# Kernel tuning notes

Measured on AMD Instinct MI355X. Metric: run time of the kernel, lower is better.

The kernel has to match this reference:

```python
import jax, jax.numpy as jnp
import numpy as np

DIM = 1024

def setup_inputs() -> dict:
    key = jax.random.key(0)
    k1, k2, k3, k4 = jax.random.split(key, 4)
    scale = 1.0 / np.sqrt(DIM)
    return {
        "segment_embeds": jax.random.normal(k1, (32, 2048, DIM), dtype=jnp.float32),
        "Wq": jax.random.normal(k2, (DIM, DIM), dtype=jnp.float32) * scale,
        "bq": jax.random.normal(k3, (DIM,), dtype=jnp.float32) * scale,
        "mem_bank": jax.random.normal(k4, (131072, DIM), dtype=jnp.float32) * scale,
        "k": 8,
    }

def reference(segment_embeds, Wq, bq, mem_bank, k):
    # mean-pool over time: (B, C)
    segment_mean = segment_embeds.mean(axis=1)
    # linear query projection (torch Linear: x @ W.T + b)
    q = segment_mean @ Wq.T + bq
    # dense scores against memory bank: (B, M)
    attn_scores = (q @ mem_bank.T) / jnp.sqrt(jnp.asarray(DIM, dtype=q.dtype))
    # top-k select
    top_k_scores, top_k_indices = jax.lax.top_k(attn_scores, k)  # (B, K)
    attn_weights = jax.nn.softmax(top_k_scores, axis=-1)  # (B, K)
    # gather retrieved vectors: (B, K, C)
    retrieved_vectors = mem_bank[top_k_indices]
    # weighted sum over K, keepdim -> (B, 1, C)
    retrieved_mem = jnp.sum(attn_weights[..., None] * retrieved_vectors, axis=1, keepdims=True)
    return retrieved_mem
```

## Files before the change

### kernel.cpp

```cpp
#include <hip/hip_runtime.h>
#include <hip/hip_bf16.h>
#include <math.h>

#define NB 32
#define NT 2048
#define NC 1024
#define NM 131072
#define TOPK 8
#define MBLK 128
#define SBLOCKS (NM / MBLK)

typedef __attribute__((ext_vector_type(8))) short s16x8;
typedef __attribute__((ext_vector_type(4))) float f32x4;
typedef __attribute__((ext_vector_type(4))) int i32x4;

#define OFF_PART 0
#define OFF_CS   0
#define OFF_CI   262144
#define OFF_MEAN 1048576
#define OFF_Q    (OFF_MEAN + 32768)
#define OFF_QB   (OFF_Q + 32768)

__device__ __forceinline__ unsigned short f2bf(float f) {
    unsigned u = __float_as_uint(f);
    unsigned r = (u + 0x7FFFu + ((u >> 16) & 1u)) >> 16;
    return (unsigned short)r;
}

__global__ __launch_bounds__(256) void mean_partial_k(const float* __restrict__ seg,
                                                      float* __restrict__ part) {
    int blk = blockIdx.x;
    int b = blk >> 5, tc = blk & 31;
    int tid = threadIdx.x;
    const float4* src = (const float4*)(seg + ((size_t)b * NT + (size_t)tc * 64) * NC);
    float4 acc = make_float4(0.f, 0.f, 0.f, 0.f);
#pragma unroll 4
    for (int t = 0; t < 64; ++t) {
        float4 v = src[(size_t)t * 256 + tid];
        acc.x += v.x; acc.y += v.y; acc.z += v.z; acc.w += v.w;
    }
    ((float4*)(part + ((size_t)b * 32 + tc) * NC))[tid] = acc;
}

__global__ __launch_bounds__(256) void mean_finalize_k(const float* __restrict__ part,
                                                       float* __restrict__ mean) {
    int i = blockIdx.x * 256 + threadIdx.x;
    int b = i >> 10, c = i & 1023;
    float s = 0.f;
#pragma unroll
    for (int tc = 0; tc < 32; ++tc) s += part[((size_t)b * 32 + tc) * NC + c];
    mean[i] = s * (1.0f / NT);
}

__global__ __launch_bounds__(256) void qproj_k(const float* __restrict__ mean,
                                               const float* __restrict__ Wq,
                                               const float* __restrict__ bq,
                                               float* __restrict__ q) {
    int wave = (blockIdx.x * 256 + threadIdx.x) >> 6;
    int lane = threadIdx.x & 63;
    int o0 = wave * 16;
    for (int j = 0; j < 16; ++j) {
        int o = o0 + j;
        int b = o >> 10, i = o & 1023;
        const float4* wr = (const float4*)(Wq + (size_t)i * NC);
        const float4* mr = (const float4*)(mean + (size_t)b * NC);
        float acc = 0.f;
#pragma unroll
        for (int e = 0; e < 4; ++e) {
            float4 w4 = wr[lane * 4 + e];
            float4 m4 = mr[lane * 4 + e];
            acc += w4.x * m4.x + w4.y * m4.y + w4.z * m4.z + w4.w * m4.w;
        }
#pragma unroll
        for (int off = 32; off; off >>= 1) acc += __shfl_xor(acc, off);
        if (lane == 0) q[o] = acc + bq[i];
    }
}

__global__ __launch_bounds__(256) void qbf_k(const float* __restrict__ q,
                                             s16x8* __restrict__ qb) {
    int idx = blockIdx.x * 256 + threadIdx.x;
    int lane = idx & 63, n = (idx >> 6) & 1, ks = idx >> 7;
    int b = n * 16 + (lane & 15);
    int k0 = ks * 32 + ((lane >> 4) << 3);
    s16x8 v;
#pragma unroll
    for (int e = 0; e < 8; ++e) v[e] = (short)f2bf(q[(size_t)b * NC + k0 + e]);
    qb[idx] = v;
}

#define BUBBLE8(v, vi, s, si)                                   \
    {                                                           \
        float _v = (v); int _vi = (vi);                         \
        _Pragma("unroll")                                       \
        for (int _u = 0; _u < 8; ++_u) {                        \
            bool _gt = _v > s[_u];                              \
            float _ts = _gt ? _v : s[_u];                       \
            int _ti = _gt ? _vi : si[_u];                       \
            _v = _gt ? s[_u] : _v;                              \
            _vi = _gt ? si[_u] : _vi;                           \
            s[_u] = _ts; si[_u] = _ti;                          \
        }                                                       \
    }

__global__ __launch_bounds__(256) void scores_mfma_k(const float* __restrict__ memb,
                                                     const s16x8* __restrict__ qb,
                                                     float* __restrict__ candS,
                                                     int* __restrict__ candI) {
    __shared__ __align__(16) float smemf[5760];
    int tid = threadIdx.x, lane = tid & 63, wid = tid >> 6;
    int m0 = blockIdx.x * MBLK;

    f32x4 acc[2][2];
#pragma unroll
    for (int t = 0; t < 2; ++t)
#pragma unroll
        for (int n = 0; n < 2; ++n)
            acc[t][n] = (f32x4){0.f, 0.f, 0.f, 0.f};

    const unsigned* abase = (const unsigned*)(memb
        + (size_t)(m0 + wid * 32 + (lane & 15)) * NC + ((lane >> 4) << 3));
    s16x8 bf0 = qb[0 * 64 + lane];
    s16x8 bf1 = qb[1 * 64 + lane];

    for (int ks = 0; ks < 32; ++ks) {
        s16x8 nb0, nb1;
        if (ks < 31) {
            nb0 = qb[((ks + 1) * 2 + 0) * 64 + lane];
            nb1 = qb[((ks + 1) * 2 + 1) * 64 + lane];
        }
#pragma unroll
        for (int t = 0; t < 2; ++t) {
            const unsigned* ap = abase + (size_t)(t * 16) * NC + ks * 32;
            uint4 lo = *(const uint4*)(ap);
            uint4 hi = *(const uint4*)(ap + 4);
            i32x4 ai;
            ai[0] = __builtin_amdgcn_perm(lo.y, lo.x, 0x07060302u);
            ai[1] = __builtin_amdgcn_perm(lo.w, lo.z, 0x07060302u);
            ai[2] = __builtin_amdgcn_perm(hi.y, hi.x, 0x07060302u);
            ai[3] = __builtin_amdgcn_perm(hi.w, hi.z, 0x07060302u);
            s16x8 a = __builtin_bit_cast(s16x8, ai);
            acc[t][0] = __builtin_amdgcn_mfma_f32_16x16x32_bf16(a, bf0, acc[t][0], 0, 0, 0);
            acc[t][1] = __builtin_amdgcn_mfma_f32_16x16x32_bf16(a, bf1, acc[t][1], 0, 0, 0);
        }
        bf0 = nb0; bf1 = nb1;
    }

#pragma unroll
    for (int t = 0; t < 2; ++t)
#pragma unroll
        for (int n = 0; n < 2; ++n)
#pragma unroll
            for (int j = 0; j < 4; ++j) {
                int bb = n * 16 + (lane & 15);
                int mm = wid * 32 + t * 16 + ((lane >> 4) << 2) + j;
                smemf[bb * 129 + mm] = acc[t][n][j] * 0.03125f;
            }
    __syncthreads();

    {
        int b = tid >> 3, p = tid & 7;
        float s[8]; int si[8];
#pragma unroll
        for (int u = 0; u < 8; ++u) { s[u] = -INFINITY; si[u] = -1; }
#pragma unroll
        for (int j = 0; j < 16; ++j) {
            int ml = (p + j * 8 + b * 4) & 127;
            float v = smemf[b * 129 + ml];
            BUBBLE8(v, m0 + ml, s, si);
        }
        __syncthreads();
        float* cs = smemf;
        int* ci = (int*)(smemf + 2304);
#pragma unroll
        for (int u = 0; u < 8; ++u) { cs[tid * 9 + u] = s[u]; ci[tid * 9 + u] = si[u]; }
        __syncthreads();
        float* csA = smemf + 4608;
        int* ciA = (int*)(smemf + 5184);
        if (tid < 64) {
            float s2[8]; int si2[8];
#pragma unroll
            for (int u = 0; u < 8; ++u) { s2[u] = -INFINITY; si2[u] = -1; }
            int t0 = (tid >> 1) * 8 + (tid & 1) * 4;
            for (int tt = 0; tt < 4; ++tt)
#pragma unroll
                for (int u = 0; u < 8; ++u)
                    BUBBLE8(cs[(t0 + tt) * 9 + u], ci[(t0 + tt) * 9 + u], s2, si2);
#pragma unroll
            for (int u = 0; u < 8; ++u) { csA[tid * 9 + u] = s2[u]; ciA[tid * 9 + u] = si2[u]; }
        }
        __syncthreads();
        if (tid < 32) {
            float s3[8]; int si3[8];
#pragma unroll
            for (int u = 0; u < 8; ++u) { s3[u] = -INFINITY; si3[u] = -1; }
            for (int j = 0; j < 16; ++j)
                BUBBLE8(csA[(tid * 2 + (j >> 3)) * 9 + (j & 7)],
                        ciA[(tid * 2 + (j >> 3)) * 9 + (j & 7)], s3, si3);
#pragma unroll
            for (int u = 0; u < 8; ++u) {
                candS[((size_t)tid * SBLOCKS + blockIdx.x) * 8 + u] = s3[u];
                candI[((size_t)tid * SBLOCKS + blockIdx.x) * 8 + u] = si3[u];
            }
        }
    }
}

__global__ __launch_bounds__(256) void finalize_k(const float* __restrict__ candS,
                                                  const int* __restrict__ candI,
                                                  const float* __restrict__ memb,
                                                  const float* __restrict__ q,
                                                  float* __restrict__ out) {
    __shared__ float cs[256 * 9];
    __shared__ int ci[256 * 9];
    __shared__ float csA[64 * 9];
    __shared__ int ciA[64 * 9];
    __shared__ float exsc[64];
    __shared__ int exid[64];
    __shared__ float wgt[8];
    __shared__ int widx[8];
    int b = blockIdx.x, tid = threadIdx.x;
    const float* S = candS + (size_t)b * (SBLOCKS * 8);
    const int* I = candI + (size_t)b * (SBLOCKS * 8);

    {
        float s[8]; int si[8];
#pragma unroll
        for (int u = 0; u < 8; ++u) { s[u] = -INFINITY; si[u] = -1; }
        for (int j = 0; j < 32; ++j)
            BUBBLE8(S[tid * 32 + j], I[tid * 32 + j], s, si);
#pragma unroll
        for (int u = 0; u < 8; ++u) { cs[tid * 9 + u] = s[u]; ci[tid * 9 + u] = si[u]; }
    }
    __syncthreads();
    if (tid < 64) {
        float s[8]; int si[8];
#pragma unroll
        for (int u = 0; u < 8; ++u) { s[u] = -INFINITY; si[u] = -1; }
        for (int tt = 0; tt < 4; ++tt)
#pragma unroll
            for (int u = 0; u < 8; ++u)
                BUBBLE8(cs[(tid * 4 + tt) * 9 + u], ci[(tid * 4 + tt) * 9 + u], s, si);
#pragma unroll
        for (int u = 0; u < 8; ++u) { csA[tid * 9 + u] = s[u]; ciA[tid * 9 + u] = si[u]; }
    }
    __syncthreads();
    if (tid < 8) {
        float s[8]; int si[8];
#pragma unroll
        for (int u = 0; u < 8; ++u) { s[u] = -INFINITY; si[u] = -1; }
        for (int tt = 0; tt < 8; ++tt)
#pragma unroll
            for (int u = 0; u < 8; ++u)
                BUBBLE8(csA[(tid * 8 + tt) * 9 + u], ciA[(tid * 8 + tt) * 9 + u], s, si);
#pragma unroll
        for (int u = 0; u < 8; ++u) exid[tid * 8 + u] = si[u];
    }
    __syncthreads();
    {
        int w = tid >> 6, lane = tid & 63;
        const float4* qr = (const float4*)(q + (size_t)b * NC);
        for (int i = 0; i < 16; ++i) {
            int c = w * 16 + i;
            int row = exid[c];
            const float4* mr = (const float4*)(memb + (size_t)row * NC);
            float d = 0.f;
#pragma unroll
            for (int e = 0; e < 4; ++e) {
                float4 m4 = mr[e * 64 + lane];
                float4 q4 = qr[e * 64 + lane];
                d += m4.x * q4.x + m4.y * q4.y + m4.z * q4.z + m4.w * q4.w;
            }
#pragma unroll
            for (int off = 32; off; off >>= 1) d += __shfl_xor(d, off);
            if (lane == 0) exsc[c] = d * 0.03125f;
        }
    }
    __syncthreads();
    if (tid == 0) {
        float s4[8]; int si4[8];
#pragma unroll
        for (int u = 0; u < 8; ++u) { s4[u] = -INFINITY; si4[u] = -1; }
        for (int j = 0; j < 64; ++j)
            BUBBLE8(exsc[j], exid[j], s4, si4);
        float m = s4[0], sum = 0.f, w[8];
#pragma unroll
        for (int u = 0; u < 8; ++u) { w[u] = __expf(s4[u] - m); sum += w[u]; }
        float inv = 1.0f / sum;
#pragma unroll
        for (int u = 0; u < 8; ++u) { wgt[u] = w[u] * inv; widx[u] = si4[u]; }
    }
    __syncthreads();
    {
        float wv[8]; int ix[8];
#pragma unroll
        for (int u = 0; u < 8; ++u) { wv[u] = wgt[u]; ix[u] = widx[u]; }
        float4 o = make_float4(0.f, 0.f, 0.f, 0.f);
#pragma unroll
        for (int u = 0; u < 8; ++u) {
            float4 r = ((const float4*)(memb + (size_t)ix[u] * NC))[tid];
            o.x = fmaf(wv[u], r.x, o.x);
            o.y = fmaf(wv[u], r.y, o.y);
            o.z = fmaf(wv[u], r.z, o.z);
            o.w = fmaf(wv[u], r.w, o.w);
        }
        ((float4*)(out + (size_t)b * NC))[tid] = o;
    }
}

extern "C" void kernel_launch(void* const* d_in, const int* in_sizes, int n_in,
                              void* d_out, int out_size, void* d_ws, size_t ws_size,
                              hipStream_t stream) {
    const float* seg  = (const float*)d_in[0];
    const float* Wq   = (const float*)d_in[1];
    const float* bq   = (const float*)d_in[2];
    const float* memb = (const float*)d_in[3];
    float* ws = (float*)d_ws;
    float* part  = ws + OFF_PART;
    float* mean  = ws + OFF_MEAN;
    float* q     = ws + OFF_Q;
    s16x8* qb    = (s16x8*)(ws + OFF_QB);
    float* candS = ws + OFF_CS;
    int*   candI = (int*)(ws + OFF_CI);
    float* out = (float*)d_out;

    mean_partial_k<<<NB * 32, 256, 0, stream>>>(seg, part);
    mean_finalize_k<<<(NB * NC) / 256, 256, 0, stream>>>(part, mean);
    qproj_k<<<512, 256, 0, stream>>>(mean, Wq, bq, q);
    qbf_k<<<16, 256, 0, stream>>>(q, qb);
    scores_mfma_k<<<SBLOCKS, 256, 0, stream>>>(memb, qb, candS, candI);
    finalize_k<<<NB, 256, 0, stream>>>(candS, candI, memb, q, out);
}
```

Measured before the change: 233.8 us.

## Halve score tile per block, pack indices into score bits, prefetch A loads

The scoring kernel now covers 64 memory rows per block instead of 128, with one 16-row MFMA tile per wave, and raises the occupancy hint to 8 blocks. The next k-step's memory-bank loads are prefetched into registers across iterations, using a scheduling barrier. The local row index is packed into the low 8 mantissa bits of each score, so the per-block top-8 selection sorts floats only and drops the parallel index arrays. This trades a tiny loss of score precision, which could change tie ordering, for fewer registers and less shared memory, while doubling the candidate count the finalize kernel has to merge.

```diff
diff --git a/kernel.cpp b/kernel.cpp
--- a/kernel.cpp
+++ b/kernel.cpp
@@ -7,7 +7,7 @@
 #define NC 1024
 #define NM 131072
 #define TOPK 8
-#define MBLK 128
+#define MBLK 64
 #define SBLOCKS (NM / MBLK)
 
 typedef __attribute__((ext_vector_type(8))) short s16x8;
@@ -16,7 +16,7 @@
 
 #define OFF_PART 0
 #define OFF_CS   0
-#define OFF_CI   262144
+#define OFF_CI   524288
 #define OFF_MEAN 1048576
 #define OFF_Q    (OFF_MEAN + 32768)
 #define OFF_QB   (OFF_Q + 32768)
@@ -103,104 +103,109 @@
         }                                                       \
     }
 
-__global__ __launch_bounds__(256) void scores_mfma_k(const float* __restrict__ memb,
-                                                     const s16x8* __restrict__ qb,
-                                                     float* __restrict__ candS,
-                                                     int* __restrict__ candI) {
-    __shared__ __align__(16) float smemf[5760];
+#define BUBBLE8F(v, s)                                          \
+    {                                                           \
+        float _v = (v);                                         \
+        _Pragma("unroll")                                       \
+        for (int _u = 0; _u < 8; ++_u) {                        \
+            bool _gt = _v > s[_u];                              \
+            float _ts = _gt ? _v : s[_u];                       \
+            _v = _gt ? s[_u] : _v;                              \
+            s[_u] = _ts;                                        \
+        }                                                       \
+    }
+
+__global__ __launch_bounds__(256, 8) void scores_mfma_k(const float* __restrict__ memb,
+                                                        const s16x8* __restrict__ qb,
+                                                        float* __restrict__ candS,
+                                                        int* __restrict__ candI) {
+    __shared__ __align__(16) float smemf[2880];
     int tid = threadIdx.x, lane = tid & 63, wid = tid >> 6;
     int m0 = blockIdx.x * MBLK;
 
-    f32x4 acc[2][2];
-#pragma unroll
-    for (int t = 0; t < 2; ++t)
-#pragma unroll
-        for (int n = 0; n < 2; ++n)
-            acc[t][n] = (f32x4){0.f, 0.f, 0.f, 0.f};
+    f32x4 acc[2];
+    acc[0] = (f32x4){0.f, 0.f, 0.f, 0.f};
+    acc[1] = (f32x4){0.f, 0.f, 0.f, 0.f};
 
     const unsigned* abase = (const unsigned*)(memb
-        + (size_t)(m0 + wid * 32 + (lane & 15)) * NC + ((lane >> 4) << 3));
-    s16x8 bf0 = qb[0 * 64 + lane];
-    s16x8 bf1 = qb[1 * 64 + lane];
+        + (size_t)(m0 + wid * 16 + (lane & 15)) * NC + ((lane >> 4) << 3));
+    uint4 lo0 = *(const uint4*)(abase);
+    uint4 hi0 = *(const uint4*)(abase + 4);
+    s16x8 bf0 = qb[lane];
+    s16x8 bf1 = qb[64 + lane];
 
     for (int ks = 0; ks < 32; ++ks) {
-        s16x8 nb0, nb1;
+        uint4 lo1, hi1; s16x8 nb0, nb1;
         if (ks < 31) {
+            lo1 = *(const uint4*)(abase + (ks + 1) * 32);
+            hi1 = *(const uint4*)(abase + (ks + 1) * 32 + 4);
             nb0 = qb[((ks + 1) * 2 + 0) * 64 + lane];
             nb1 = qb[((ks + 1) * 2 + 1) * 64 + lane];
         }
-#pragma unroll
-        for (int t = 0; t < 2; ++t) {
-            const unsigned* ap = abase + (size_t)(t * 16) * NC + ks * 32;
-            uint4 lo = *(const uint4*)(ap);
-            uint4 hi = *(const uint4*)(ap + 4);
-            i32x4 ai;
-            ai[0] = __builtin_amdgcn_perm(lo.y, lo.x, 0x07060302u);
-            ai[1] = __builtin_amdgcn_perm(lo.w, lo.z, 0x07060302u);
-            ai[2] = __builtin_amdgcn_perm(hi.y, hi.x, 0x07060302u);
-            ai[3] = __builtin_amdgcn_perm(hi.w, hi.z, 0x07060302u);
-            s16x8 a = __builtin_bit_cast(s16x8, ai);
-            acc[t][0] = __builtin_amdgcn_mfma_f32_16x16x32_bf16(a, bf0, acc[t][0], 0, 0, 0);
-            acc[t][1] = __builtin_amdgcn_mfma_f32_16x16x32_bf16(a, bf1, acc[t][1], 0, 0, 0);
-        }
-        bf0 = nb0; bf1 = nb1;
-    }
-
-#pragma unroll
-    for (int t = 0; t < 2; ++t)
-#pragma unroll
-        for (int n = 0; n < 2; ++n)
-#pragma unroll
-            for (int j = 0; j < 4; ++j) {
-                int bb = n * 16 + (lane & 15);
-                int mm = wid * 32 + t * 16 + ((lane >> 4) << 2) + j;
-                smemf[bb * 129 + mm] = acc[t][n][j] * 0.03125f;
-            }
+        __builtin_amdgcn_sched_barrier(0);
+        i32x4 ai;
+        ai[0] = __builtin_amdgcn_perm(lo0.y, lo0.x, 0x07060302u);
+        ai[1] = __builtin_amdgcn_perm(lo0.w, lo0.z, 0x07060302u);
+        ai[2] = __builtin_amdgcn_perm(hi0.y, hi0.x, 0x07060302u);
+        ai[3] = __builtin_amdgcn_perm(hi0.w, hi0.z, 0x07060302u);
+        s16x8 a = __builtin_bit_cast(s16x8, ai);
+        acc[0] = __builtin_amdgcn_mfma_f32_16x16x32_bf16(a, bf0, acc[0], 0, 0, 0);
+        acc[1] = __builtin_amdgcn_mfma_f32_16x16x32_bf16(a, bf1, acc[1], 0, 0, 0);
+        lo0 = lo1; hi0 = hi1; bf0 = nb0; bf1 = nb1;
+    }
+
+#pragma unroll
+    for (int n = 0; n < 2; ++n)
+#pragma unroll
+        for (int j = 0; j < 4; ++j) {
+            int bb = n * 16 + (lane & 15);
+            int mm = wid * 16 + ((lane >> 4) << 2) + j;
+            smemf[bb * 65 + mm] = acc[n][j] * 0.03125f;
+        }
     __syncthreads();
 
     {
         int b = tid >> 3, p = tid & 7;
-        float s[8]; int si[8];
-#pragma unroll
-        for (int u = 0; u < 8; ++u) { s[u] = -INFINITY; si[u] = -1; }
-#pragma unroll
-        for (int j = 0; j < 16; ++j) {
-            int ml = (p + j * 8 + b * 4) & 127;
-            float v = smemf[b * 129 + ml];
-            BUBBLE8(v, m0 + ml, s, si);
+        float s[8];
+#pragma unroll
+        for (int u = 0; u < 8; ++u) s[u] = -INFINITY;
+#pragma unroll
+        for (int j = 0; j < 8; ++j) {
+            int ml = (p + j * 8 + b * 4) & 63;
+            float v = smemf[b * 65 + ml];
+            unsigned uu = (__float_as_uint(v) & ~0xFFu) | (unsigned)ml;
+            BUBBLE8F(__uint_as_float(uu), s);
         }
         __syncthreads();
         float* cs = smemf;
-        int* ci = (int*)(smemf + 2304);
-#pragma unroll
-        for (int u = 0; u < 8; ++u) { cs[tid * 9 + u] = s[u]; ci[tid * 9 + u] = si[u]; }
+#pragma unroll
+        for (int u = 0; u < 8; ++u) cs[tid * 9 + u] = s[u];
         __syncthreads();
-        float* csA = smemf + 4608;
-        int* ciA = (int*)(smemf + 5184);
+        float* csA = smemf + 2304;
         if (tid < 64) {
-            float s2[8]; int si2[8];
-#pragma unroll
-            for (int u = 0; u < 8; ++u) { s2[u] = -INFINITY; si2[u] = -1; }
+            float s2[8];
+#pragma unroll
+            for (int u = 0; u < 8; ++u) s2[u] = -INFINITY;
             int t0 = (tid >> 1) * 8 + (tid & 1) * 4;
             for (int tt = 0; tt < 4; ++tt)
 #pragma unroll
                 for (int u = 0; u < 8; ++u)
-                    BUBBLE8(cs[(t0 + tt) * 9 + u], ci[(t0 + tt) * 9 + u], s2, si2);
-#pragma unroll
-            for (int u = 0; u < 8; ++u) { csA[tid * 9 + u] = s2[u]; ciA[tid * 9 + u] = si2[u]; }
+                    BUBBLE8F(cs[(t0 + tt) * 9 + u], s2);
+#pragma unroll
+            for (int u = 0; u < 8; ++u) csA[tid * 9 + u] = s2[u];
         }
         __syncthreads();
         if (tid < 32) {
-            float s3[8]; int si3[8];
-#pragma unroll
-            for (int u = 0; u < 8; ++u) { s3[u] = -INFINITY; si3[u] = -1; }
+            float s3[8];
+#pragma unroll
+            for (int u = 0; u < 8; ++u) s3[u] = -INFINITY;
             for (int j = 0; j < 16; ++j)
-                BUBBLE8(csA[(tid * 2 + (j >> 3)) * 9 + (j & 7)],
-                        ciA[(tid * 2 + (j >> 3)) * 9 + (j & 7)], s3, si3);
+                BUBBLE8F(csA[(tid * 2 + (j >> 3)) * 9 + (j & 7)], s3);
 #pragma unroll
             for (int u = 0; u < 8; ++u) {
                 candS[((size_t)tid * SBLOCKS + blockIdx.x) * 8 + u] = s3[u];
-                candI[((size_t)tid * SBLOCKS + blockIdx.x) * 8 + u] = si3[u];
+                candI[((size_t)tid * SBLOCKS + blockIdx.x) * 8 + u] =
+                    m0 + (int)(__float_as_uint(s3[u]) & 0xFFu);
             }
         }
     }
@@ -227,8 +232,8 @@
         float s[8]; int si[8];
 #pragma unroll
         for (int u = 0; u < 8; ++u) { s[u] = -INFINITY; si[u] = -1; }
-        for (int j = 0; j < 32; ++j)
-            BUBBLE8(S[tid * 32 + j], I[tid * 32 + j], s, si);
+        for (int j = 0; j < 64; ++j)
+            BUBBLE8(S[tid * 64 + j], I[tid * 64 + j], s, si);
 #pragma unroll
         for (int u = 0; u < 8; ++u) { cs[tid * 9 + u] = s[u]; ci[tid * 9 + u] = si[u]; }
     }
```

New measurement: 233.2 us. About the same (-0.3%).

## Restructure scores kernel into single-wave blocks with double-buffered LDS staging

Applied to the files above, without the earlier changes.

The memory-bank scoring kernel now runs as 1024 single-wavefront blocks. Each block walks 8 panels of 16 rows and double-buffers 16x256 float tiles into LDS with direct global-to-LDS loads, prefetching the next tile while the MFMAs run on the current one. Top-k is kept per lane across panels and merged with a shuffle instead of multi-stage shared-memory reductions with block barriers. The goal is to overlap the bank streaming with compute and drop the synchronization overhead. In exchange there is less parallelism per block, explicit vmcnt(0) waits that may serialize the loads, and q fragments re-read from global on every tile.

```diff
diff --git a/kernel.cpp b/kernel.cpp
--- a/kernel.cpp
+++ b/kernel.cpp
@@ -7,8 +7,9 @@
 #define NC 1024
 #define NM 131072
 #define TOPK 8
-#define MBLK 128
-#define SBLOCKS (NM / MBLK)
+#define PANELS 8
+#define NSB 1024
+#define SLOTF 260
 
 typedef __attribute__((ext_vector_type(8))) short s16x8;
 typedef __attribute__((ext_vector_type(4))) float f32x4;
@@ -25,6 +26,11 @@
     unsigned u = __float_as_uint(f);
     unsigned r = (u + 0x7FFFu + ((u >> 16) & 1u)) >> 16;
     return (unsigned short)r;
+}
+
+__device__ __forceinline__ void gl_lds16(const float* g, float* l) {
+    __builtin_amdgcn_global_load_lds((const __attribute__((address_space(1))) void*)g,
+                                     (__attribute__((address_space(3))) void*)l, 16, 0, 0);
 }
 
 __global__ __launch_bounds__(256) void mean_partial_k(const float* __restrict__ seg,
@@ -94,7 +100,7 @@
         float _v = (v); int _vi = (vi);                         \
         _Pragma("unroll")                                       \
         for (int _u = 0; _u < 8; ++_u) {                        \
-            bool _gt = _v > s[_u];                              \
+            bool _gt = _v > s[_u];                               \
             float _ts = _gt ? _v : s[_u];                       \
             int _ti = _gt ? _vi : si[_u];                       \
             _v = _gt ? s[_u] : _v;                              \
@@ -103,104 +109,98 @@
         }                                                       \
     }
 
-__global__ __launch_bounds__(256) void scores_mfma_k(const float* __restrict__ memb,
-                                                     const s16x8* __restrict__ qb,
-                                                     float* __restrict__ candS,
-                                                     int* __restrict__ candI) {
-    __shared__ __align__(16) float smemf[5760];
-    int tid = threadIdx.x, lane = tid & 63, wid = tid >> 6;
-    int m0 = blockIdx.x * MBLK;
-
-    f32x4 acc[2][2];
-#pragma unroll
-    for (int t = 0; t < 2; ++t)
-#pragma unroll
-        for (int n = 0; n < 2; ++n)
-            acc[t][n] = (f32x4){0.f, 0.f, 0.f, 0.f};
-
-    const unsigned* abase = (const unsigned*)(memb
-        + (size_t)(m0 + wid * 32 + (lane & 15)) * NC + ((lane >> 4) << 3));
-    s16x8 bf0 = qb[0 * 64 + lane];
-    s16x8 bf1 = qb[1 * 64 + lane];
-
-    for (int ks = 0; ks < 32; ++ks) {
-        s16x8 nb0, nb1;
-        if (ks < 31) {
-            nb0 = qb[((ks + 1) * 2 + 0) * 64 + lane];
-            nb1 = qb[((ks + 1) * 2 + 1) * 64 + lane];
-        }
-#pragma unroll
-        for (int t = 0; t < 2; ++t) {
-            const unsigned* ap = abase + (size_t)(t * 16) * NC + ks * 32;
-            uint4 lo = *(const uint4*)(ap);
-            uint4 hi = *(const uint4*)(ap + 4);
+__global__ __launch_bounds__(64) void scores_mfma_k(const float* __restrict__ memb,
+                                                    const s16x8* __restrict__ qb,
+                                                    float* __restrict__ candS,
+                                                    int* __restrict__ candI) {
+    __shared__ __align__(16) float tiles[2 * 16 * SLOTF];
+    __shared__ __align__(16) float sc[32 * 17];
+    int lane = threadIdx.x;
+    size_t mb0 = (size_t)blockIdx.x * (PANELS * 16);
+
+    float s8[8]; int i8[8];
+#pragma unroll
+    for (int u = 0; u < 8; ++u) { s8[u] = -INFINITY; i8[u] = -1; }
+
+#define TISSUE(t_) { int p_ = (t_) >> 2, c_ = (t_) & 3;                               \
+    const float* rb_ = memb + (mb0 + p_ * 16) * NC + c_ * 256 + lane * 4;             \
+    float* lb_ = tiles + ((t_) & 1) * (16 * SLOTF);                                   \
+    _Pragma("unroll") for (int i_ = 0; i_ < 16; ++i_)                                 \
+        gl_lds16(rb_ + (size_t)i_ * NC, lb_ + i_ * SLOTF); }
+
+    f32x4 acc0 = (f32x4){0.f, 0.f, 0.f, 0.f};
+    f32x4 acc1 = (f32x4){0.f, 0.f, 0.f, 0.f};
+
+    TISSUE(0);
+    for (int t = 0; t < PANELS * 4; ++t) {
+        int c = t & 3;
+        s16x8 qf[16];
+#pragma unroll
+        for (int k = 0; k < 8; ++k) {
+            qf[2 * k]     = qb[((c * 8 + k) * 2 + 0) * 64 + lane];
+            qf[2 * k + 1] = qb[((c * 8 + k) * 2 + 1) * 64 + lane];
+        }
+        asm volatile("s_waitcnt vmcnt(0)" ::: "memory");
+        __builtin_amdgcn_sched_barrier(0);
+        if (t + 1 < PANELS * 4) TISSUE(t + 1);
+
+        const float* lanebase = tiles + (t & 1) * (16 * SLOTF)
+                              + (lane & 15) * SLOTF + ((lane >> 4) << 3);
+#pragma unroll
+        for (int ks = 0; ks < 8; ++ks) {
+            uint4 lo = *(const uint4*)(lanebase + ks * 32);
+            uint4 hi = *(const uint4*)(lanebase + ks * 32 + 4);
             i32x4 ai;
             ai[0] = __builtin_amdgcn_perm(lo.y, lo.x, 0x07060302u);
             ai[1] = __builtin_amdgcn_perm(lo.w, lo.z, 0x07060302u);
             ai[2] = __builtin_amdgcn_perm(hi.y, hi.x, 0x07060302u);
             ai[3] = __builtin_amdgcn_perm(hi.w, hi.z, 0x07060302u);
             s16x8 a = __builtin_bit_cast(s16x8, ai);
-            acc[t][0] = __builtin_amdgcn_mfma_f32_16x16x32_bf16(a, bf0, acc[t][0], 0, 0, 0);
-            acc[t][1] = __builtin_amdgcn_mfma_f32_16x16x32_bf16(a, bf1, acc[t][1], 0, 0, 0);
-        }
-        bf0 = nb0; bf1 = nb1;
-    }
-
-#pragma unroll
-    for (int t = 0; t < 2; ++t)
-#pragma unroll
-        for (int n = 0; n < 2; ++n)
+            acc0 = __builtin_amdgcn_mfma_f32_16x16x32_bf16(a, qf[2 * ks], acc0, 0, 0, 0);
+            acc1 = __builtin_amdgcn_mfma_f32_16x16x32_bf16(a, qf[2 * ks + 1], acc1, 0, 0, 0);
+        }
+
+        if (c == 3) {
+            int p = t >> 2;
 #pragma unroll
             for (int j = 0; j < 4; ++j) {
-                int bb = n * 16 + (lane & 15);
-                int mm = wid * 32 + t * 16 + ((lane >> 4) << 2) + j;
-                smemf[bb * 129 + mm] = acc[t][n][j] * 0.03125f;
+                sc[(0 * 16 + (lane & 15)) * 17 + ((lane >> 4) << 2) + j] = acc0[j];
+                sc[(1 * 16 + (lane & 15)) * 17 + ((lane >> 4) << 2) + j] = acc1[j];
             }
-    __syncthreads();
+            asm volatile("s_waitcnt lgkmcnt(0)" ::: "memory");
+            __builtin_amdgcn_sched_barrier(0);
+            int b = lane >> 1, p2 = lane & 1;
+            int midx0 = mb0 + p * 16;
+#pragma unroll
+            for (int j = 0; j < 8; ++j) {
+                int m = ((b + j) & 7) + p2 * 8;
+                float v = sc[b * 17 + m];
+                BUBBLE8(v, midx0 + m, s8, i8);
+            }
+            asm volatile("s_waitcnt lgkmcnt(0)" ::: "memory");
+            __builtin_amdgcn_sched_barrier(0);
+            acc0 = (f32x4){0.f, 0.f, 0.f, 0.f};
+            acc1 = (f32x4){0.f, 0.f, 0.f, 0.f};
+        }
+    }
+#undef TISSUE
 
     {
-        int b = tid >> 3, p = tid & 7;
-        float s[8]; int si[8];
-#pragma unroll
-        for (int u = 0; u < 8; ++u) { s[u] = -INFINITY; si[u] = -1; }
-#pragma unroll
-        for (int j = 0; j < 16; ++j) {
-            int ml = (p + j * 8 + b * 4) & 127;
-            float v = smemf[b * 129 + ml];
-            BUBBLE8(v, m0 + ml, s, si);
-        }
-        __syncthreads();
-        float* cs = smemf;
-        int* ci = (int*)(smemf + 2304);
-#pragma unroll
-        for (int u = 0; u < 8; ++u) { cs[tid * 9 + u] = s[u]; ci[tid * 9 + u] = si[u]; }
-        __syncthreads();
-        float* csA = smemf + 4608;
-        int* ciA = (int*)(smemf + 5184);
-        if (tid < 64) {
-            float s2[8]; int si2[8];
-#pragma unroll
-            for (int u = 0; u < 8; ++u) { s2[u] = -INFINITY; si2[u] = -1; }
-            int t0 = (tid >> 1) * 8 + (tid & 1) * 4;
-            for (int tt = 0; tt < 4; ++tt)
-#pragma unroll
-                for (int u = 0; u < 8; ++u)
-                    BUBBLE8(cs[(t0 + tt) * 9 + u], ci[(t0 + tt) * 9 + u], s2, si2);
-#pragma unroll
-            for (int u = 0; u < 8; ++u) { csA[tid * 9 + u] = s2[u]; ciA[tid * 9 + u] = si2[u]; }
-        }
-        __syncthreads();
-        if (tid < 32) {
-            float s3[8]; int si3[8];
-#pragma unroll
-            for (int u = 0; u < 8; ++u) { s3[u] = -INFINITY; si3[u] = -1; }
-            for (int j = 0; j < 16; ++j)
-                BUBBLE8(csA[(tid * 2 + (j >> 3)) * 9 + (j & 7)],
-                        ciA[(tid * 2 + (j >> 3)) * 9 + (j & 7)], s3, si3);
+        float ov[8]; int oi[8];
+#pragma unroll
+        for (int u = 0; u < 8; ++u) { ov[u] = s8[u]; oi[u] = i8[u]; }
+#pragma unroll
+        for (int u = 0; u < 8; ++u) {
+            float pv = __shfl_xor(ov[u], 1);
+            int pi = __shfl_xor(oi[u], 1);
+            BUBBLE8(pv, pi, s8, i8);
+        }
+        if ((lane & 1) == 0) {
+            int b = lane >> 1;
 #pragma unroll
             for (int u = 0; u < 8; ++u) {
-                candS[((size_t)tid * SBLOCKS + blockIdx.x) * 8 + u] = s3[u];
-                candI[((size_t)tid * SBLOCKS + blockIdx.x) * 8 + u] = si3[u];
+                candS[(size_t)b * (NSB * 8) + blockIdx.x * 8 + u] = s8[u] * 0.03125f;
+                candI[(size_t)b * (NSB * 8) + blockIdx.x * 8 + u] = i8[u];
             }
         }
     }
@@ -220,8 +220,8 @@
     __shared__ float wgt[8];
     __shared__ int widx[8];
     int b = blockIdx.x, tid = threadIdx.x;
-    const float* S = candS + (size_t)b * (SBLOCKS * 8);
-    const int* I = candI + (size_t)b * (SBLOCKS * 8);
+    const float* S = candS + (size_t)b * (NSB * 8);
+    const int* I = candI + (size_t)b * (NSB * 8);
 
     {
         float s[8]; int si[8];
@@ -328,6 +328,6 @@
     mean_finalize_k<<<(NB * NC) / 256, 256, 0, stream>>>(part, mean);
     qproj_k<<<512, 256, 0, stream>>>(mean, Wq, bq, q);
     qbf_k<<<16, 256, 0, stream>>>(q, qb);
-    scores_mfma_k<<<SBLOCKS, 256, 0, stream>>>(memb, qb, candS, candI);
+    scores_mfma_k<<<NSB, 64, 0, stream>>>(memb, qb, candS, candI);
     finalize_k<<<NB, 256, 0, stream>>>(candS, candI, memb, q, out);
 }
```

After: 213.6 us. 1.09x faster.
